# Optimization experiments

Measured on AMD Instinct MI355X. Metric: run time of the kernel, lower is better.

Reference implementation:

```python
import jax, jax.numpy as jnp
import numpy as np

B, T, D, H = 32, 512, 512, 512


def _run_dir(x, W, b, reverse):
    # W: [D+H, 4H] packed gate weights in order [i, f, o, g]; b: [4H]
    Wx, Wh = W[:D], W[D:]
    # Precompute input contribution to all gates for all timesteps at once.
    xp = jnp.einsum('btd,dk->btk', x, Wx) + b  # [B, T, 4H]

    def step(carry, xt):
        h, c = carry
        z = xt + h @ Wh  # [B, 4H]
        i_t, f_t, o_t, g_t = jnp.split(z, 4, axis=-1)
        c = jax.nn.sigmoid(f_t) * c + jax.nn.sigmoid(i_t) * jnp.tanh(g_t)
        h = jax.nn.sigmoid(o_t) * jnp.tanh(c)
        return (h, c), h

    init = (jnp.zeros((x.shape[0], H), x.dtype), jnp.zeros((x.shape[0], H), x.dtype))
    _, hs = jax.lax.scan(step, init, xp.swapaxes(0, 1), reverse=reverse)  # [T, B, H]
    return hs.swapaxes(0, 1)  # [B, T, H]


def setup_inputs() -> dict:
    key = jax.random.key(0)
    ks = jax.random.split(key, 5)
    s_w = 1.0 / np.sqrt(D + H)
    x = jax.random.normal(ks[0], (B, T, D), dtype=jnp.float32)
    W_fw = jax.random.normal(ks[1], (D + H, 4 * H), dtype=jnp.float32) * s_w
    b_fw = jax.random.normal(ks[2], (4 * H,), dtype=jnp.float32) * s_w
    W_bw = jax.random.normal(ks[3], (D + H, 4 * H), dtype=jnp.float32) * s_w
    b_bw = jax.random.normal(ks[4], (4 * H,), dtype=jnp.float32) * s_w
    return {"x": x, "W_fw": W_fw, "b_fw": b_fw, "W_bw": W_bw, "b_bw": b_bw}


def reference(x, W_fw, b_fw, W_bw, b_bw):
    h_fw = _run_dir(x, W_fw, b_fw, reverse=False)
    h_bw = _run_dir(x, W_bw, b_bw, reverse=True)
    return jnp.concatenate([h_fw, h_bw], axis=-1)  # [B, T, 2H]
```

## Files before the change

kernel.cpp:

```cpp
#include <hip/hip_runtime.h>
#include <hip/hip_bf16.h>

#define Bz 32
#define Tz 512
#define Dz 512
#define Hz 512
#define NG 4
#define GWG 32
#define ROWS 16
#define COLS 16

typedef __attribute__((ext_vector_type(8))) short short8;
typedef __attribute__((ext_vector_type(4))) short short4v;
typedef __attribute__((ext_vector_type(4))) float f32x4;

#define HBUF (ROWS * Hz * 2)
#define FLGB 512
#define WS_FLG 0
#define WS_H   (NG * FLGB)
#define WS_X   (WS_H + NG * 2 * HBUF)
#define WS_NEED ((size_t)WS_X + (size_t)Bz * Tz * Dz * 2)

__device__ __forceinline__ unsigned short f2bf(float f) {
    return __builtin_bit_cast(unsigned short, __float2bfloat16(f));
}
__device__ __forceinline__ float rcp_(float x) { return __builtin_amdgcn_rcpf(x); }
__device__ __forceinline__ float fsig(float x) { return rcp_(1.0f + __expf(-x)); }
__device__ __forceinline__ float ftanh(float x) {
    float t = __expf(-2.0f * fabsf(x));
    return copysignf((1.0f - t) * rcp_(1.0f + t), x);
}
__device__ __forceinline__ short8 mk8(unsigned long long lo, unsigned long long hi) {
    short4v a = __builtin_bit_cast(short4v, lo);
    short4v b = __builtin_bit_cast(short4v, hi);
    short8 r;
    r[0]=a[0]; r[1]=a[1]; r[2]=a[2]; r[3]=a[3];
    r[4]=b[0]; r[5]=b[1]; r[6]=b[2]; r[7]=b[3];
    return r;
}

__global__ void init_kernel(const float* __restrict__ x, unsigned char* __restrict__ ws, int do_x) {
    int tid = blockIdx.x * blockDim.x + threadIdx.x;
    unsigned int* w32 = (unsigned int*)ws;
    if (tid < (WS_X / 4)) w32[tid] = 0u;
    if (do_x) {
        const int n4 = (Bz * Tz * Dz) / 4;
        if (tid < n4) {
            const float4* xin = (const float4*)x;
            float4 v = xin[tid];
            unsigned int u0 = (unsigned)f2bf(v.x) | ((unsigned)f2bf(v.y) << 16);
            unsigned int u1 = (unsigned)f2bf(v.z) | ((unsigned)f2bf(v.w) << 16);
            unsigned int* xo = (unsigned int*)(ws + WS_X);
            xo[tid * 2]     = u0;
            xo[tid * 2 + 1] = u1;
        }
    }
}

template <bool XB>
__launch_bounds__(256, 1)
__global__ void lstm_kernel(const float* __restrict__ xf,
                            const float* __restrict__ Wf, const float* __restrict__ bf,
                            const float* __restrict__ Wb, const float* __restrict__ bb,
                            float* __restrict__ out, unsigned char* __restrict__ ws) {
    const int bi   = blockIdx.x;
    const int dir  = bi & 1;
    const int grp  = (bi >> 1) & 1;
    const int wg   = bi >> 2;
    const int gid  = dir * 2 + grp;
    const int j0   = wg * COLS;
    const int b0   = grp * ROWS;
    const int tid  = threadIdx.x;
    const int wave = tid >> 6;
    const int lane = tid & 63;
    const int nidx = lane & 15;
    const int quad = lane >> 4;

    const float* W    = dir ? Wb : Wf;
    const float* bias = dir ? bb : bf;

    unsigned int* flg = (unsigned int*)(ws + WS_FLG + gid * FLGB);
    unsigned char* hbase = ws + WS_H + gid * 2 * HBUF;
    const unsigned short* xbf = (const unsigned short*)(ws + WS_X);

    __shared__ float part[4][4][16][17];

    short8 bfrag[8][4];
    {
        const int krow0 = (wave < 2) ? wave * 256 : 512 + (wave - 2) * 256;
        #pragma unroll
        for (int i = 0; i < 8; ++i) {
            #pragma unroll
            for (int g = 0; g < 4; ++g) {
                short8 v;
                #pragma unroll
                for (int jj = 0; jj < 8; ++jj) {
                    int krow = krow0 + i * 32 + quad * 8 + jj;
                    v[jj] = (short)f2bf(W[krow * (4 * Hz) + g * 512 + j0 + nidx]);
                }
                bfrag[i][g] = v;
            }
        }
    }

    const int erow = tid >> 4;
    const int ecol = tid & 15;
    float bia[4];
    #pragma unroll
    for (int g = 0; g < 4; ++g) bia[g] = bias[g * 512 + j0 + ecol];
    float creg = 0.f;
    const size_t outbase = ((size_t)(b0 + erow) * Tz) * (2 * Hz) + dir * Hz + j0 + ecol;

    int par = 0;
    for (int s = 0; s < Tz; ++s) {
        const int t = dir ? (Tz - 1 - s) : s;
        f32x4 acc[4] = {{0,0,0,0},{0,0,0,0},{0,0,0,0},{0,0,0,0}};

        if (wave < 2) {
            const int kb = wave * 256;
            short8 a[8];
            if (XB) {
                #pragma unroll
                for (int i = 0; i < 8; ++i) {
                    int k = kb + i * 32 + quad * 8;
                    a[i] = *(const short8*)(xbf + (((b0 + nidx) * Tz + t) * Dz + k));
                }
            } else {
                #pragma unroll
                for (int i = 0; i < 8; ++i) {
                    int k = kb + i * 32 + quad * 8;
                    const float* q = xf + (((b0 + nidx) * Tz + t) * Dz + k);
                    short8 sv;
                    #pragma unroll
                    for (int jj = 0; jj < 8; ++jj) sv[jj] = (short)f2bf(q[jj]);
                    a[i] = sv;
                }
            }
            #pragma unroll
            for (int i = 0; i < 8; ++i)
                #pragma unroll
                for (int g = 0; g < 4; ++g)
                    acc[g] = __builtin_amdgcn_mfma_f32_16x16x32_bf16(a[i], bfrag[i][g], acc[g], 0, 0, 0);
        } else {
            {
                const unsigned tgt = (unsigned)s;
                const int fi = (lane & 31) * 4;
                for (;;) {
                    unsigned f = __hip_atomic_load(flg + fi, __ATOMIC_RELAXED, __HIP_MEMORY_SCOPE_AGENT);
                    if (__ballot(f >= tgt) == ~0ull) break;
                    __builtin_amdgcn_s_sleep(1);
                }
            }
            const unsigned long long* hb = (const unsigned long long*)(hbase + par * HBUF);
            const int kb = (wave - 2) * 256;
            short8 a[8];
            #pragma unroll
            for (int i = 0; i < 8; ++i) {
                int k  = kb + i * 32 + quad * 8;
                int i0 = (nidx * Hz + k) >> 2;
                unsigned long long l0 = __hip_atomic_load(hb + i0,     __ATOMIC_RELAXED, __HIP_MEMORY_SCOPE_AGENT);
                unsigned long long l1 = __hip_atomic_load(hb + i0 + 1, __ATOMIC_RELAXED, __HIP_MEMORY_SCOPE_AGENT);
                a[i] = mk8(l0, l1);
            }
            #pragma unroll
            for (int i = 0; i < 8; ++i)
                #pragma unroll
                for (int g = 0; g < 4; ++g)
                    acc[g] = __builtin_amdgcn_mfma_f32_16x16x32_bf16(a[i], bfrag[i][g], acc[g], 0, 0, 0);
        }

        {
            const int r0 = quad * 4;
            #pragma unroll
            for (int g = 0; g < 4; ++g)
                #pragma unroll
                for (int r = 0; r < 4; ++r)
                    part[wave][g][r0 + r][nidx] = acc[g][r];
        }
        __syncthreads();

        float hv;
        {
            float z[4];
            #pragma unroll
            for (int g = 0; g < 4; ++g)
                z[g] = bia[g] + part[0][g][erow][ecol] + part[1][g][erow][ecol]
                             + part[2][g][erow][ecol] + part[3][g][erow][ecol];
            float c = fsig(z[1]) * creg + fsig(z[0]) * ftanh(z[3]);
            creg = c;
            hv = fsig(z[2]) * ftanh(c);
            float hp = __shfl_xor(hv, 1);
            if ((ecol & 1) == 0) {
                unsigned d = (unsigned)f2bf(hv) | ((unsigned)f2bf(hp) << 16);
                unsigned* hw = (unsigned*)(hbase + (par ^ 1) * HBUF);
                __hip_atomic_store(hw + erow * (Hz / 2) + ((j0 + ecol) >> 1), d,
                                   __ATOMIC_RELAXED, __HIP_MEMORY_SCOPE_AGENT);
            }
        }

        asm volatile("s_waitcnt vmcnt(0)" ::: "memory");
        __syncthreads();
        if (tid == 0)
            __hip_atomic_store(flg + wg * 4, (unsigned)(s + 1),
                               __ATOMIC_RELAXED, __HIP_MEMORY_SCOPE_AGENT);
        out[outbase + (size_t)t * (2 * Hz)] = hv;
        par ^= 1;
    }
}

extern "C" void kernel_launch(void* const* d_in, const int* in_sizes, int n_in,
                              void* d_out, int out_size, void* d_ws, size_t ws_size,
                              hipStream_t stream) {
    const float* x  = (const float*)d_in[0];
    const float* Wf = (const float*)d_in[1];
    const float* bf = (const float*)d_in[2];
    const float* Wb = (const float*)d_in[3];
    const float* bb = (const float*)d_in[4];
    float* out = (float*)d_out;
    unsigned char* ws = (unsigned char*)d_ws;
    const bool xb = (ws_size >= WS_NEED);

    init_kernel<<<8192, 256, 0, stream>>>(x, ws, xb ? 1 : 0);
    if (xb)
        lstm_kernel<true><<<NG * GWG, 256, 0, stream>>>(x, Wf, bf, Wb, bb, out, ws);
    else
        lstm_kernel<false><<<NG * GWG, 256, 0, stream>>>(x, Wf, bf, Wb, bb, out, ws);
}
```

Baseline: 1.968 ms.

## Replace per-step flag barrier with step-tagged hidden-state words polled directly

Each hidden value is now stored as a 32-bit word carrying the bf16 value in the low half and the step number in the high half. Consumers poll the hidden buffer itself until every tag matches the current step. This removes the separate flag array, the vmcnt drain, the second __syncthreads and the flag store per step, and double-buffers the LDS partial-sum array so only one block barrier remains per step. In exchange the h buffer doubles in size, so each step reads twice as many bytes over the recurrence path, and the atomic loads are re-issued on every poll.

```diff
diff --git a/kernel.cpp b/kernel.cpp
--- a/kernel.cpp
+++ b/kernel.cpp
@@ -11,14 +11,12 @@
 #define COLS 16
 
 typedef __attribute__((ext_vector_type(8))) short short8;
-typedef __attribute__((ext_vector_type(4))) short short4v;
 typedef __attribute__((ext_vector_type(4))) float f32x4;
-
-#define HBUF (ROWS * Hz * 2)
-#define FLGB 512
-#define WS_FLG 0
-#define WS_H   (NG * FLGB)
-#define WS_X   (WS_H + NG * 2 * HBUF)
+typedef __attribute__((ext_vector_type(4))) unsigned int u32x4;
+
+#define HBUF (ROWS * Hz * 4)
+#define WS_H 0
+#define WS_X (NG * 2 * HBUF)
 #define WS_NEED ((size_t)WS_X + (size_t)Bz * Tz * Dz * 2)
 
 __device__ __forceinline__ unsigned short f2bf(float f) {
@@ -29,14 +27,6 @@
 __device__ __forceinline__ float ftanh(float x) {
     float t = __expf(-2.0f * fabsf(x));
     return copysignf((1.0f - t) * rcp_(1.0f + t), x);
-}
-__device__ __forceinline__ short8 mk8(unsigned long long lo, unsigned long long hi) {
-    short4v a = __builtin_bit_cast(short4v, lo);
-    short4v b = __builtin_bit_cast(short4v, hi);
-    short8 r;
-    r[0]=a[0]; r[1]=a[1]; r[2]=a[2]; r[3]=a[3];
-    r[4]=b[0]; r[5]=b[1]; r[6]=b[2]; r[7]=b[3];
-    return r;
 }
 
 __global__ void init_kernel(const float* __restrict__ x, unsigned char* __restrict__ ws, int do_x) {
@@ -79,11 +69,10 @@
     const float* W    = dir ? Wb : Wf;
     const float* bias = dir ? bb : bf;
 
-    unsigned int* flg = (unsigned int*)(ws + WS_FLG + gid * FLGB);
     unsigned char* hbase = ws + WS_H + gid * 2 * HBUF;
     const unsigned short* xbf = (const unsigned short*)(ws + WS_X);
 
-    __shared__ float part[4][4][16][17];
+    __shared__ float part[2][4][4][16][17];
 
     short8 bfrag[8][4];
     {
@@ -111,9 +100,9 @@
     float creg = 0.f;
     const size_t outbase = ((size_t)(b0 + erow) * Tz) * (2 * Hz) + dir * Hz + j0 + ecol;
 
-    int par = 0;
     for (int s = 0; s < Tz; ++s) {
-        const int t = dir ? (Tz - 1 - s) : s;
+        const int t   = dir ? (Tz - 1 - s) : s;
+        const int par = s & 1;
         f32x4 acc[4] = {{0,0,0,0},{0,0,0,0},{0,0,0,0},{0,0,0,0}};
 
         if (wave < 2) {
@@ -142,25 +131,30 @@
                 for (int g = 0; g < 4; ++g)
                     acc[g] = __builtin_amdgcn_mfma_f32_16x16x32_bf16(a[i], bfrag[i][g], acc[g], 0, 0, 0);
         } else {
-            {
-                const unsigned tgt = (unsigned)s;
-                const int fi = (lane & 31) * 4;
-                for (;;) {
-                    unsigned f = __hip_atomic_load(flg + fi, __ATOMIC_RELAXED, __HIP_MEMORY_SCOPE_AGENT);
-                    if (__ballot(f >= tgt) == ~0ull) break;
-                    __builtin_amdgcn_s_sleep(1);
-                }
-            }
-            const unsigned long long* hb = (const unsigned long long*)(hbase + par * HBUF);
             const int kb = (wave - 2) * 256;
+            const unsigned long long* hb64 = (const unsigned long long*)(hbase + par * HBUF);
+            const unsigned txor = ((unsigned)s) << 16;
             short8 a[8];
-            #pragma unroll
-            for (int i = 0; i < 8; ++i) {
-                int k  = kb + i * 32 + quad * 8;
-                int i0 = (nidx * Hz + k) >> 2;
-                unsigned long long l0 = __hip_atomic_load(hb + i0,     __ATOMIC_RELAXED, __HIP_MEMORY_SCOPE_AGENT);
-                unsigned long long l1 = __hip_atomic_load(hb + i0 + 1, __ATOMIC_RELAXED, __HIP_MEMORY_SCOPE_AGENT);
-                a[i] = mk8(l0, l1);
+            for (;;) {
+                unsigned bad = 0;
+                #pragma unroll
+                for (int i = 0; i < 8; ++i) {
+                    const int k = kb + i * 32 + quad * 8;
+                    const unsigned long long* p = hb64 + ((nidx * Hz + k) >> 1);
+                    u32x4 w;
+                    #pragma unroll
+                    for (int q = 0; q < 4; ++q) {
+                        unsigned long long r = __hip_atomic_load(p + q, __ATOMIC_RELAXED, __HIP_MEMORY_SCOPE_AGENT);
+                        unsigned lo = (unsigned)r;
+                        unsigned hi = (unsigned)(r >> 32);
+                        bad |= lo ^ txor;
+                        bad |= hi ^ txor;
+                        w[q] = __builtin_amdgcn_perm(hi, lo, 0x05040100u);
+                    }
+                    a[i] = __builtin_bit_cast(short8, w);
+                }
+                if (__ballot((bad >> 16) == 0) == ~0ull) break;
+                __builtin_amdgcn_s_sleep(1);
             }
             #pragma unroll
             for (int i = 0; i < 8; ++i)
@@ -175,36 +169,25 @@
             for (int g = 0; g < 4; ++g)
                 #pragma unroll
                 for (int r = 0; r < 4; ++r)
-                    part[wave][g][r0 + r][nidx] = acc[g][r];
+                    part[par][wave][g][r0 + r][nidx] = acc[g][r];
         }
         __syncthreads();
 
-        float hv;
         {
             float z[4];
             #pragma unroll
             for (int g = 0; g < 4; ++g)
-                z[g] = bia[g] + part[0][g][erow][ecol] + part[1][g][erow][ecol]
-                             + part[2][g][erow][ecol] + part[3][g][erow][ecol];
+                z[g] = bia[g] + part[par][0][g][erow][ecol] + part[par][1][g][erow][ecol]
+                             + part[par][2][g][erow][ecol] + part[par][3][g][erow][ecol];
             float c = fsig(z[1]) * creg + fsig(z[0]) * ftanh(z[3]);
             creg = c;
-            hv = fsig(z[2]) * ftanh(c);
-            float hp = __shfl_xor(hv, 1);
-            if ((ecol & 1) == 0) {
-                unsigned d = (unsigned)f2bf(hv) | ((unsigned)f2bf(hp) << 16);
-                unsigned* hw = (unsigned*)(hbase + (par ^ 1) * HBUF);
-                __hip_atomic_store(hw + erow * (Hz / 2) + ((j0 + ecol) >> 1), d,
-                                   __ATOMIC_RELAXED, __HIP_MEMORY_SCOPE_AGENT);
-            }
-        }
-
-        asm volatile("s_waitcnt vmcnt(0)" ::: "memory");
-        __syncthreads();
-        if (tid == 0)
-            __hip_atomic_store(flg + wg * 4, (unsigned)(s + 1),
+            float hv = fsig(z[2]) * ftanh(c);
+            unsigned* hw = (unsigned*)(hbase + (par ^ 1) * HBUF);
+            unsigned d = (unsigned)f2bf(hv) | ((unsigned)(s + 1) << 16);
+            __hip_atomic_store(hw + erow * Hz + (j0 + ecol), d,
                                __ATOMIC_RELAXED, __HIP_MEMORY_SCOPE_AGENT);
-        out[outbase + (size_t)t * (2 * Hz)] = hv;
-        par ^= 1;
+            out[outbase + (size_t)t * (2 * Hz)] = hv;
+        }
     }
 }
 
```

After: 4.790 ms. +143.3%, slower.

## Replace second block barrier with LDS handshake and double-buffer partials

Applied to the files above, without the earlier changes.

The gate epilogue now runs only on the two x-waves, two columns per thread. Those waves signal completion through an LDS atomic counter instead of a second __syncthreads, so the h-waves can start spinning on the next step's flag sooner. The partial-sum buffer is double-buffered by step parity to avoid overwrite races, and the sleep in the spin loop is removed to cut wake-up latency. The catch is more epilogue work per thread, plus spin-loop pressure on the LDS and memory system.

```diff
diff --git a/kernel.cpp b/kernel.cpp
--- a/kernel.cpp
+++ b/kernel.cpp
@@ -83,7 +83,9 @@
     unsigned char* hbase = ws + WS_H + gid * 2 * HBUF;
     const unsigned short* xbf = (const unsigned short*)(ws + WS_X);
 
-    __shared__ float part[4][4][16][17];
+    __shared__ float part[2][4][4][16][17];
+    __shared__ int hsk;
+    if (tid == 0) hsk = 0;
 
     short8 bfrag[8][4];
     {
@@ -103,17 +105,22 @@
         }
     }
 
-    const int erow = tid >> 4;
-    const int ecol = tid & 15;
-    float bia[4];
-    #pragma unroll
-    for (int g = 0; g < 4; ++g) bia[g] = bias[g * 512 + j0 + ecol];
-    float creg = 0.f;
-    const size_t outbase = ((size_t)(b0 + erow) * Tz) * (2 * Hz) + dir * Hz + j0 + ecol;
-
-    int par = 0;
+    const int erow = tid >> 3;
+    const int ec2  = (tid & 7) * 2;
+    float bia[4][2];
+    float creg[2] = {0.f, 0.f};
+    if (wave < 2) {
+        #pragma unroll
+        for (int g = 0; g < 4; ++g) {
+            bia[g][0] = bias[g * 512 + j0 + ec2];
+            bia[g][1] = bias[g * 512 + j0 + ec2 + 1];
+        }
+    }
+    const size_t outbase = ((size_t)(b0 + erow) * Tz) * (2 * Hz) + dir * Hz + j0 + ec2;
+
     for (int s = 0; s < Tz; ++s) {
-        const int t = dir ? (Tz - 1 - s) : s;
+        const int t   = dir ? (Tz - 1 - s) : s;
+        const int par = s & 1;
         f32x4 acc[4] = {{0,0,0,0},{0,0,0,0},{0,0,0,0},{0,0,0,0}};
 
         if (wave < 2) {
@@ -144,11 +151,10 @@
         } else {
             {
                 const unsigned tgt = (unsigned)s;
-                const int fi = (lane & 31) * 4;
+                const int fi = ((wave - 2) * 16 + (lane & 15)) * 4;
                 for (;;) {
                     unsigned f = __hip_atomic_load(flg + fi, __ATOMIC_RELAXED, __HIP_MEMORY_SCOPE_AGENT);
                     if (__ballot(f >= tgt) == ~0ull) break;
-                    __builtin_amdgcn_s_sleep(1);
                 }
             }
             const unsigned long long* hb = (const unsigned long long*)(hbase + par * HBUF);
@@ -175,36 +181,38 @@
             for (int g = 0; g < 4; ++g)
                 #pragma unroll
                 for (int r = 0; r < 4; ++r)
-                    part[wave][g][r0 + r][nidx] = acc[g][r];
+                    part[par][wave][g][r0 + r][nidx] = acc[g][r];
         }
         __syncthreads();
 
-        float hv;
-        {
-            float z[4];
-            #pragma unroll
-            for (int g = 0; g < 4; ++g)
-                z[g] = bia[g] + part[0][g][erow][ecol] + part[1][g][erow][ecol]
-                             + part[2][g][erow][ecol] + part[3][g][erow][ecol];
-            float c = fsig(z[1]) * creg + fsig(z[0]) * ftanh(z[3]);
-            creg = c;
-            hv = fsig(z[2]) * ftanh(c);
-            float hp = __shfl_xor(hv, 1);
-            if ((ecol & 1) == 0) {
-                unsigned d = (unsigned)f2bf(hv) | ((unsigned)f2bf(hp) << 16);
+        if (wave < 2) {
+            float hv[2];
+            #pragma unroll
+            for (int c = 0; c < 2; ++c) {
+                float z[4];
+                #pragma unroll
+                for (int g = 0; g < 4; ++g)
+                    z[g] = bia[g][c] + part[par][0][g][erow][ec2 + c] + part[par][1][g][erow][ec2 + c]
+                                     + part[par][2][g][erow][ec2 + c] + part[par][3][g][erow][ec2 + c];
+                float c_ = fsig(z[1]) * creg[c] + fsig(z[0]) * ftanh(z[3]);
+                creg[c] = c_;
+                hv[c] = fsig(z[2]) * ftanh(c_);
+            }
+            {
+                unsigned d = (unsigned)f2bf(hv[0]) | ((unsigned)f2bf(hv[1]) << 16);
                 unsigned* hw = (unsigned*)(hbase + (par ^ 1) * HBUF);
-                __hip_atomic_store(hw + erow * (Hz / 2) + ((j0 + ecol) >> 1), d,
+                __hip_atomic_store(hw + erow * (Hz / 2) + ((j0 + ec2) >> 1), d,
                                    __ATOMIC_RELAXED, __HIP_MEMORY_SCOPE_AGENT);
             }
-        }
-
-        asm volatile("s_waitcnt vmcnt(0)" ::: "memory");
-        __syncthreads();
-        if (tid == 0)
-            __hip_atomic_store(flg + wg * 4, (unsigned)(s + 1),
-                               __ATOMIC_RELAXED, __HIP_MEMORY_SCOPE_AGENT);
-        out[outbase + (size_t)t * (2 * Hz)] = hv;
-        par ^= 1;
+            asm volatile("s_waitcnt vmcnt(0)" ::: "memory");
+            if (lane == 0) atomicAdd(&hsk, 1);
+            if (tid == 0) {
+                while (__hip_atomic_load(&hsk, __ATOMIC_RELAXED, __HIP_MEMORY_SCOPE_WORKGROUP) < 2 * (s + 1)) {}
+                __hip_atomic_store(flg + wg * 4, (unsigned)(s + 1),
+                                   __ATOMIC_RELAXED, __HIP_MEMORY_SCOPE_AGENT);
+            }
+            *(float2*)(out + outbase + (size_t)t * (2 * Hz)) = make_float2(hv[0], hv[1]);
+        }
     }
 }
 
```

After: 2.145 ms. 9.0% more time.
